# Performance work log

Hardware: AMD Instinct MI355X
Metric: run time of the kernel (lower is better)

## Reference

```python
import jax, jax.numpy as jnp
import numpy as np

V, N, D, HEADS = 4, 1536, 256, 4


def setup_inputs() -> dict:
    key = jax.random.key(0)
    ks = jax.random.split(key, 8)
    s = 0.05  # weight init scale
    return {
        "H": jax.random.normal(ks[0], (V, N, D), jnp.float32),
        "C": jax.random.normal(ks[1], (V, V, N, N), jnp.float32),
        "WQ": jax.random.normal(ks[2], (V, D, D), jnp.float32) * s,
        "WK": jax.random.normal(ks[3], (V, D, D), jnp.float32) * s,
        "WV": jax.random.normal(ks[4], (V, D, D), jnp.float32) * s,
        "in_proj_w": jax.random.normal(ks[5], (3 * D, D), jnp.float32) * s,
        "in_proj_b": jnp.zeros((3 * D,), jnp.float32),
        "out_proj_w": jax.random.normal(ks[6], (D, D), jnp.float32) * s,
        "out_proj_b": jnp.zeros((D,), jnp.float32),
        "alphas": jnp.full((V,), 0.95, jnp.float32),
        "alpha_align": jnp.asarray(0.5, jnp.float32),
        "beta": jnp.asarray(0.5, jnp.float32),
        "topk": 32,
    }


def _ircva(H, in_proj_w, in_proj_b, out_proj_w, out_proj_b, alphas):
    # torch MultiheadAttention, seq=V, batch=N, embed=D, heads=HEADS
    dh = D // HEADS
    qkv = jnp.einsum('snd,ed->sne', H, in_proj_w) + in_proj_b  # (V,N,3D)
    q, k, v = jnp.split(qkv, 3, axis=-1)
    q = q.reshape(V, N, HEADS, dh)
    k = k.reshape(V, N, HEADS, dh)
    v = v.reshape(V, N, HEADS, dh)
    att = jnp.einsum('snhd,tnhd->nhst', q, k) / jnp.sqrt(jnp.float32(dh))
    w = jax.nn.softmax(att, axis=-1)
    o = jnp.einsum('nhst,tnhd->snhd', w, v).reshape(V, N, D)
    fusion = jnp.einsum('snd,ed->sne', o, out_proj_w) + out_proj_b
    a = alphas[:, None, None]
    return fusion * a + (1.0 - a) * H  # (V,N,D)


def _crcva(aligned, C, WQ, WK, WV, K):
    # per-view projections: Linear y = x @ W.T
    Qn = jnp.einsum('vnd,ved->vne', aligned, WQ)
    Kn = jnp.einsum('vnd,ved->vne', aligned, WK)
    Vn = jnp.einsum('vnd,ved->vne', aligned, WV)
    # per-row top-k sparsification of C[p,q]
    vals, idx = jax.lax.top_k(C, K)  # (V,V,N,K)
    Cf = C.reshape(-1, N)
    rows = jnp.arange(Cf.shape[0])[:, None]
    sparse = jnp.zeros_like(Cf).at[rows, idx.reshape(-1, K)].set(vals.reshape(-1, K))
    sparse = sparse.reshape(V, V, N, N)
    row_sum = sparse.sum(axis=-1, keepdims=True) + 1e-12
    C_hat = sparse / row_sum
    # diagonal (p==q) pairs are left as zeros in the torch code
    offdiag = (1.0 - jnp.eye(V, dtype=C.dtype))[:, :, None, None]
    C_hat = C_hat * offdiag
    mask = (C_hat > 0).astype(C.dtype)
    scores = jnp.einsum('pnd,qmd->pqnm', Qn, Kn) / jnp.sqrt(jnp.float32(D))
    scores = scores * mask + (1.0 - mask) * (-1e9)
    alpha_nbr = jax.nn.softmax(scores, axis=-1)
    return jnp.einsum('pqnm,qmd->pnd', alpha_nbr, Vn)  # (V,N,D)


def reference(H, C, WQ, WK, WV, in_proj_w, in_proj_b, out_proj_w, out_proj_b,
              alphas, alpha_align, beta, topk):
    aligned = _ircva(H, in_proj_w, in_proj_b, out_proj_w, out_proj_b, alphas)
    nbr = _crcva(aligned, C, WQ, WK, WV, int(topk))
    a = jax.nn.sigmoid(alpha_align)
    f_fuse = jax.nn.relu(a * aligned + (1.0 - a) * nbr)
    return beta * H + (1.0 - beta) * f_fuse  # (V,N,D)
```

## Files before the change

kernel.cpp:

```cpp
#include <hip/hip_runtime.h>
#include <hip/hip_bf16.h>
#include <math.h>

typedef __bf16 bf16x8 __attribute__((ext_vector_type(8)));
typedef __bf16 bf16x4 __attribute__((ext_vector_type(4)));
typedef float  f32x4  __attribute__((ext_vector_type(4)));

static constexpr int kV = 4;
static constexpr int kN = 1536;
static constexpr int kD = 256;
static constexpr int kTopK = 32;

__global__ __launch_bounds__(256) void convert_kernel(
    const float* __restrict__ H, const float* __restrict__ inW,
    const float* __restrict__ outW, const float* __restrict__ WQ,
    const float* __restrict__ WK, const float* __restrict__ WV,
    __bf16* __restrict__ Hb, __bf16* __restrict__ inWb,
    __bf16* __restrict__ outWb, __bf16* __restrict__ Wqkvb,
    float* __restrict__ Vmean)
{
    if (blockIdx.x == 0) {
        f32x4 z = {0.f, 0.f, 0.f, 0.f};
        *(f32x4*)(Vmean + threadIdx.x * 4) = z;
    }
    int idx = (blockIdx.x * 256 + threadIdx.x) * 4;
    const float* src; __bf16* dst; int off;
    if      (idx < 1572864) { src = H;    dst = Hb;             off = idx; }
    else if (idx < 1769472) { src = inW;  dst = inWb;           off = idx - 1572864; }
    else if (idx < 1835008) { src = outW; dst = outWb;          off = idx - 1769472; }
    else if (idx < 2097152) { src = WQ;   dst = Wqkvb;          off = idx - 1835008; }
    else if (idx < 2359296) { src = WK;   dst = Wqkvb + 262144; off = idx - 2097152; }
    else                    { src = WV;   dst = Wqkvb + 524288; off = idx - 2359296; }
    f32x4 v = *(const f32x4*)(src + off);
    bf16x4 b;
#pragma unroll
    for (int j = 0; j < 4; ++j) b[j] = (__bf16)v[j];
    *(bf16x4*)(dst + off) = b;
}

__global__ __launch_bounds__(256) void gemm_qkv_kernel(
    const __bf16* __restrict__ A, const __bf16* __restrict__ Bm,
    const float* __restrict__ bias, __bf16* __restrict__ outB)
{
    const int Nc = 768, K = 256;
    int wave = blockIdx.x * 4 + (threadIdx.x >> 6);
    int tm  = wave / 12;
    int tn4 = wave - tm * 12;
    int lane = threadIdx.x & 63;
    int r    = lane & 15;
    int quad = lane >> 4;
    const __bf16* Ap = A + (size_t)(tm * 32 + r) * K + quad * 8;
    const __bf16* Bp = Bm + (size_t)(tn4 * 64 + r) * K + quad * 8;
    f32x4 acc[2][4] = {};
    for (int k0 = 0; k0 < K; k0 += 32) {
        bf16x8 a0 = *(const bf16x8*)(Ap + k0);
        bf16x8 a1 = *(const bf16x8*)(Ap + (size_t)16 * K + k0);
#pragma unroll
        for (int t = 0; t < 4; ++t) {
            bf16x8 b = *(const bf16x8*)(Bp + (size_t)t * 16 * K + k0);
            acc[0][t] = __builtin_amdgcn_mfma_f32_16x16x32_bf16(a0, b, acc[0][t], 0, 0, 0);
            acc[1][t] = __builtin_amdgcn_mfma_f32_16x16x32_bf16(a1, b, acc[1][t], 0, 0, 0);
        }
    }
#pragma unroll
    for (int t = 0; t < 4; ++t) {
        int gn = tn4 * 64 + t * 16 + r;
        float bv = bias[gn];
#pragma unroll
        for (int mt = 0; mt < 2; ++mt)
#pragma unroll
            for (int i = 0; i < 4; ++i) {
                int gm = tm * 32 + mt * 16 + quad * 4 + i;
                outB[(size_t)gm * Nc + gn] = (__bf16)(acc[mt][t][i] + bv);
            }
    }
}

__global__ __launch_bounds__(256) void attg3_kernel(
    const __bf16* __restrict__ qkv, const __bf16* __restrict__ outWb,
    const float* __restrict__ outBias, const float* __restrict__ H,
    const float* __restrict__ alphas,
    float* __restrict__ alignedF, __bf16* __restrict__ alignedB)
{
    __shared__ __bf16 obuf[16][280];
    int n0 = blockIdx.x * 4;
    int tid = threadIdx.x;
    int h = tid >> 6, d = tid & 63;
#pragma unroll
    for (int ni = 0; ni < 4; ++ni) {
        int n = n0 + ni;
        float q[4], k[4], vv[4];
#pragma unroll
        for (int s = 0; s < 4; ++s) {
            size_t base = (size_t)(s * kN + n) * 768 + h * 64 + d;
            q[s]  = (float)qkv[base];
            k[s]  = (float)qkv[base + 256];
            vv[s] = (float)qkv[base + 512];
        }
        float att[4][4];
#pragma unroll
        for (int s = 0; s < 4; ++s)
#pragma unroll
            for (int t = 0; t < 4; ++t) {
                float p = q[s] * k[t];
#pragma unroll
                for (int off = 32; off > 0; off >>= 1) p += __shfl_xor(p, off);
                att[s][t] = p * 0.125f;
            }
#pragma unroll
        for (int s = 0; s < 4; ++s) {
            float mx = fmaxf(fmaxf(att[s][0], att[s][1]), fmaxf(att[s][2], att[s][3]));
            float e0 = __expf(att[s][0] - mx), e1 = __expf(att[s][1] - mx);
            float e2 = __expf(att[s][2] - mx), e3 = __expf(att[s][3] - mx);
            float inv = 1.f / (e0 + e1 + e2 + e3);
            float ov = (e0 * vv[0] + e1 * vv[1] + e2 * vv[2] + e3 * vv[3]) * inv;
            obuf[s * 4 + ni][h * 64 + d] = (__bf16)ov;
        }
    }
    __syncthreads();
    int w = tid >> 6, lane = tid & 63;
    int r = lane & 15, quad = lane >> 4;
    f32x4 acc[4] = {};
    for (int k0 = 0; k0 < 256; k0 += 32) {
        bf16x8 a = *(const bf16x8*)&obuf[r][quad * 8 + k0];
#pragma unroll
        for (int t = 0; t < 4; ++t) {
            bf16x8 b = *(const bf16x8*)(outWb + (size_t)(w * 64 + t * 16 + r) * 256 + quad * 8 + k0);
            acc[t] = __builtin_amdgcn_mfma_f32_16x16x32_bf16(a, b, acc[t], 0, 0, 0);
        }
    }
#pragma unroll
    for (int t = 0; t < 4; ++t) {
        int gn = w * 64 + t * 16 + r;
        float bv = outBias[gn];
#pragma unroll
        for (int i = 0; i < 4; ++i) {
            int rl = quad * 4 + i;
            int s = rl >> 2, ni = rl & 3;
            size_t gr = (size_t)(s * kN + n0 + ni);
            float a_ = alphas[s];
            size_t off = gr * kD + gn;
            float res = a_ * (acc[t][i] + bv) + (1.f - a_) * H[off];
            alignedF[off] = res;
            alignedB[off] = (__bf16)res;
        }
    }
}

__global__ __launch_bounds__(256) void gemm_qkv3_kernel(
    const __bf16* __restrict__ A, const __bf16* __restrict__ W,
    __bf16* __restrict__ O0, __bf16* __restrict__ O1, __bf16* __restrict__ O2,
    float* __restrict__ Vmean)
{
    int proj = blockIdx.y;
    __bf16* Ob = (proj == 0) ? O0 : (proj == 1) ? O1 : O2;
    const __bf16* Wb = W + (size_t)proj * 4 * 65536;
    int b = blockIdx.x;
    int view = b / 48;
    int tn4 = threadIdx.x >> 6;
    int lane = threadIdx.x & 63;
    int r = lane & 15, quad = lane >> 4;
    const __bf16* Ap = A + (size_t)(b * 32 + r) * kD + quad * 8;
    const __bf16* Bp = Wb + (size_t)view * 65536 + (size_t)(tn4 * 64 + r) * kD + quad * 8;
    f32x4 acc[2][4] = {};
    for (int k0 = 0; k0 < kD; k0 += 32) {
        bf16x8 a0 = *(const bf16x8*)(Ap + k0);
        bf16x8 a1 = *(const bf16x8*)(Ap + (size_t)16 * kD + k0);
#pragma unroll
        for (int t = 0; t < 4; ++t) {
            bf16x8 bb = *(const bf16x8*)(Bp + (size_t)t * 16 * kD + k0);
            acc[0][t] = __builtin_amdgcn_mfma_f32_16x16x32_bf16(a0, bb, acc[0][t], 0, 0, 0);
            acc[1][t] = __builtin_amdgcn_mfma_f32_16x16x32_bf16(a1, bb, acc[1][t], 0, 0, 0);
        }
    }
#pragma unroll
    for (int t = 0; t < 4; ++t) {
        int gn = tn4 * 64 + t * 16 + r;
#pragma unroll
        for (int mt = 0; mt < 2; ++mt)
#pragma unroll
            for (int i = 0; i < 4; ++i) {
                int gm = b * 32 + mt * 16 + quad * 4 + i;
                Ob[(size_t)gm * kD + gn] = (__bf16)acc[mt][t][i];
            }
    }
    if (proj == 2) {
#pragma unroll
        for (int t = 0; t < 4; ++t) {
            float cs = 0.f;
#pragma unroll
            for (int mt = 0; mt < 2; ++mt)
#pragma unroll
                for (int i = 0; i < 4; ++i) cs += acc[mt][t][i];
            cs += __shfl_xor(cs, 16);
            cs += __shfl_xor(cs, 32);
            if (quad == 0)
                atomicAdd(&Vmean[view * kD + tn4 * 64 + t * 16 + r], cs * (1.f / 1536.f));
        }
    }
}

__global__ __launch_bounds__(256) void crcva_kernel(
    const float* __restrict__ C,
    const __bf16* __restrict__ Qn, const __bf16* __restrict__ Kn,
    const __bf16* __restrict__ Vn, const float* __restrict__ Vmean,
    const float* __restrict__ alignedF, const float* __restrict__ H,
    const float* __restrict__ alpha_align, const float* __restrict__ beta,
    float* __restrict__ out)
{
    int gid = blockIdx.x;
    int j8  = gid & 7;
    int p   = j8 & 3;
    int n   = ((gid >> 3) << 1) | (j8 >> 2);
    int tid = threadIdx.x;
    int w = tid >> 6, lane = tid & 63;
    __shared__ unsigned int hist[3][257];
    __shared__ unsigned int sbin[3];
    __shared__ unsigned int idxl[3][kTopK];
    __shared__ unsigned int scnt[3];
    __shared__ float qsh[kD];
    __shared__ float wsh[96];
    __shared__ int   osh[96];
    __shared__ float part[4][kD];

    size_t eoff = ((size_t)p * kN + n) * kD + tid;
    float pre_al = alignedF[eoff];
    float pre_h  = H[eoff];
    float pre_vm = Vmean[p * kD + tid];
    float pre_aa = alpha_align[0];
    float pre_bt = beta[0];

    if (w < 3) {
        int q = w + (w >= p ? 1 : 0);
        const float* row = C + ((size_t)((p * kV + q) * kN + n)) * kN;
        unsigned int key[24];
#pragma unroll
        for (int j = 0; j < 6; ++j) {
            f32x4 v4 = __builtin_nontemporal_load((const f32x4*)(row + j * 256 + lane * 4));
#pragma unroll
            for (int e = 0; e < 4; ++e) {
                unsigned int u = __float_as_uint(v4[e]);
                key[j * 4 + e] = (u & 0x80000000u) ? ~u : (u | 0x80000000u);
            }
        }
        if (lane == 0) scnt[w] = 0;
        const unsigned int T0 = 0xBFCCCCCDu;
        unsigned int cand = 0;
#pragma unroll
        for (int j = 0; j < 24; ++j) cand |= (key[j] > T0) ? (1u << j) : 0u;
        unsigned int myc = (unsigned int)__popc(cand);
#pragma unroll
        for (int off = 1; off < 64; off <<= 1) myc += __shfl_xor(myc, off);
        if (myc < kTopK) {
            cand = 0;
#pragma unroll
            for (int j = 0; j < 24; ++j) cand |= (key[j] > 0x80000000u) ? (1u << j) : 0u;
        }
        unsigned int pref = 0, need = kTopK;
#pragma unroll
        for (int pass = 0; pass < 4; ++pass) {
            const int shift = 24 - 8 * pass;
#pragma unroll
            for (int k2 = 0; k2 < 4; ++k2) hist[w][lane * 4 + k2] = 0;
            if (lane == 0) sbin[w] = 0;
            __builtin_amdgcn_wave_barrier();
#pragma unroll
            for (int j = 0; j < 24; ++j) {
                unsigned int k = key[j];
                bool match = ((cand >> j) & 1u) &&
                             ((pass == 0) || (((k ^ pref) >> (shift + 8)) == 0));
                if (match) atomicAdd(&hist[w][(k >> shift) & 255u], 1u);
            }
            __builtin_amdgcn_wave_barrier();
            unsigned int h0 = hist[w][lane*4+0], h1 = hist[w][lane*4+1];
            unsigned int h2 = hist[w][lane*4+2], h3 = hist[w][lane*4+3];
            unsigned int s3 = h3, s2 = h2 + s3, s1 = h1 + s2, s0 = h0 + s1;
            unsigned int run = s0;
#pragma unroll
            for (int off = 1; off < 64; off <<= 1) {
                unsigned int v = __shfl_down(run, off);
                if (lane + off < 64) run += v;
            }
            if (pass == 0) {
                unsigned int tot = __shfl(run, 0);
                need = need < tot ? need : tot;
            }
            unsigned int above = run - s0;
            unsigned int suf[4]  = {above+s0, above+s1, above+s2, above+s3};
            unsigned int sufN[4] = {above+s1, above+s2, above+s3, above};
#pragma unroll
            for (int k2 = 0; k2 < 4; ++k2)
                if (suf[k2] >= need && sufN[k2] < need)
                    sbin[w] = ((unsigned int)(lane*4 + k2) << 16) | sufN[k2];
            __builtin_amdgcn_wave_barrier();
            unsigned int pk = sbin[w];
            pref |= (pk >> 16) << shift;
            need -= (pk & 0xffffu);
            __builtin_amdgcn_wave_barrier();
        }
        unsigned int T = pref;
        unsigned int eq = 0;
#pragma unroll
        for (int j = 0; j < 24; ++j)
            eq += (((cand >> j) & 1u) && key[j] == T) ? 1u : 0u;
#pragma unroll
        for (int off = 1; off < 64; off <<= 1) eq += __shfl_xor(eq, off);
        if (eq == need) {
#pragma unroll
            for (int j = 0; j < 24; ++j) {
                if (((cand >> j) & 1u) && key[j] >= T) {
                    unsigned int pos = atomicAdd(&scnt[w], 1u);
                    idxl[w][pos] = (unsigned int)((j >> 2) * 256 + lane * 4 + (j & 3));
                }
            }
        } else {
            unsigned int eqBefore = 0;
            unsigned long long below = (1ull << lane) - 1ull;
            for (int j4 = 0; j4 < 6; ++j4) {
                unsigned long long m[4];
#pragma unroll
                for (int e = 0; e < 4; ++e)
                    m[e] = __ballot(((cand >> (j4*4+e)) & 1u) && key[j4 * 4 + e] == T);
#pragma unroll
                for (int e = 0; e < 4; ++e) {
                    unsigned int k = key[j4 * 4 + e];
                    bool inc = (cand >> (j4*4+e)) & 1u;
                    unsigned int rank = eqBefore;
#pragma unroll
                    for (int e2 = 0; e2 < 4; ++e2) rank += (unsigned int)__popcll(m[e2] & below);
                    for (int e2 = 0; e2 < e; ++e2) rank += (unsigned int)((m[e2] >> lane) & 1ull);
                    bool iseq = inc && (k == T);
                    bool take = (inc && k > T) || (iseq && rank < need);
                    if (take) {
                        unsigned int pos = atomicAdd(&scnt[w], 1u);
                        idxl[w][pos] = (unsigned int)(j4 * 256 + lane * 4 + e);
                    }
                }
                eqBefore += (unsigned int)(__popcll(m[0]) + __popcll(m[1])
                                         + __popcll(m[2]) + __popcll(m[3]));
            }
        }
    } else {
        bf16x4 qv = *(const bf16x4*)(Qn + ((size_t)p * kN + n) * kD + lane * 4);
#pragma unroll
        for (int e = 0; e < 4; ++e) qsh[lane * 4 + e] = (float)qv[e];
    }
    __syncthreads();

    if (tid < 192) {
        int j = tid >> 1, half = tid & 1;
        int g = j >> 5, r = j & 31;
        int q = g + (g >= p ? 1 : 0);
        int cnt = (int)scnt[g];
        bool valid = (r < cnt);
        int m = valid ? (int)idxl[g][r] : 0;
        int off = valid ? (q * kN + m) * kD : 0;
        float s = 0.f;
        if (valid) {
            const __bf16* kr = Kn + off + half * 128;
            const float*  qh = qsh + half * 128;
            float a0 = 0.f, a1 = 0.f, a2 = 0.f, a3 = 0.f;
#pragma unroll
            for (int dd = 0; dd < 128; dd += 32) {
                bf16x8 k0 = *(const bf16x8*)(kr + dd);
                bf16x8 k1 = *(const bf16x8*)(kr + dd + 8);
                bf16x8 k2 = *(const bf16x8*)(kr + dd + 16);
                bf16x8 k3 = *(const bf16x8*)(kr + dd + 24);
                const float* q0 = qh + dd;
#pragma unroll
                for (int e = 0; e < 8; ++e) {
                    a0 += q0[e]      * (float)k0[e];
                    a1 += q0[e + 8]  * (float)k1[e];
                    a2 += q0[e + 16] * (float)k2[e];
                    a3 += q0[e + 24] * (float)k3[e];
                }
            }
            s = (a0 + a1) + (a2 + a3);
        }
        s += __shfl_xor(s, 1);
        float sc = valid ? s * 0.0625f : -1e30f;
        float mx = sc;
#pragma unroll
        for (int o2 = 2; o2 <= 32; o2 <<= 1) mx = fmaxf(mx, __shfl_xor(mx, o2));
        float e = valid ? __expf(sc - mx) : 0.f;
        float ss = e;
#pragma unroll
        for (int o2 = 2; o2 <= 32; o2 <<= 1) ss += __shfl_xor(ss, o2);
        if (half == 0) {
            wsh[j] = (ss > 0.f) ? e / ss : 0.f;
            osh[j] = off;
        }
    }
    __syncthreads();

    {
        int half32 = lane >> 5, l32 = lane & 31;
        float a[8] = {};
#pragma unroll
        for (int it = 0; it < 12; ++it) {
            int j = w * 24 + it * 2 + half32;
            float wt = wsh[j];
            bf16x8 v = *(const bf16x8*)(Vn + osh[j] + l32 * 8);
#pragma unroll
            for (int e = 0; e < 8; ++e) a[e] += wt * (float)v[e];
        }
#pragma unroll
        for (int e = 0; e < 8; ++e) a[e] += __shfl_xor(a[e], 32);
        if (half32 == 0) {
#pragma unroll
            for (int e = 0; e < 8; ++e) part[w][l32 * 8 + e] = a[e];
        }
    }
    __syncthreads();

    float acc = pre_vm + part[0][tid] + part[1][tid] + part[2][tid] + part[3][tid];
    float aa = 1.f / (1.f + __expf(-pre_aa));
    float f  = fmaxf(aa * pre_al + (1.f - aa) * acc, 0.f);
    out[eoff] = pre_h * pre_bt + (1.f - pre_bt) * f;
}

extern "C" void kernel_launch(void* const* d_in, const int* in_sizes, int n_in,
                              void* d_out, int out_size, void* d_ws, size_t ws_size,
                              hipStream_t stream)
{
    const float* H        = (const float*)d_in[0];
    const float* C        = (const float*)d_in[1];
    const float* WQ       = (const float*)d_in[2];
    const float* WK       = (const float*)d_in[3];
    const float* WV       = (const float*)d_in[4];
    const float* inW      = (const float*)d_in[5];
    const float* inB      = (const float*)d_in[6];
    const float* outW     = (const float*)d_in[7];
    const float* outBias  = (const float*)d_in[8];
    const float* alphas   = (const float*)d_in[9];
    const float* alpha_al = (const float*)d_in[10];
    const float* beta     = (const float*)d_in[11];
    float* out = (float*)d_out;

    char* w = (char*)d_ws;
    __bf16* Hb       = (__bf16*)w;  w += (size_t)6144 * 256 * 2;
    __bf16* inWb     = (__bf16*)w;  w += (size_t)768 * 256 * 2;
    __bf16* outWb    = (__bf16*)w;  w += (size_t)256 * 256 * 2;
    __bf16* Wqkvb    = (__bf16*)w;  w += (size_t)3 * 4 * 256 * 256 * 2;
    __bf16* qkv      = (__bf16*)w;  w += (size_t)6144 * 768 * 2;
    __bf16* alignedB = (__bf16*)w;  w += (size_t)6144 * 256 * 2;
    float*  alignedF = (float*)w;   w += (size_t)6144 * 256 * 4;
    __bf16* Qn       = (__bf16*)w;  w += (size_t)6144 * 256 * 2;
    __bf16* Kn       = (__bf16*)w;  w += (size_t)6144 * 256 * 2;
    __bf16* Vn       = (__bf16*)w;  w += (size_t)6144 * 256 * 2;
    float*  Vmean    = (float*)w;   w += (size_t)4 * 256 * 4;

    convert_kernel<<<2560, 256, 0, stream>>>(H, inW, outW, WQ, WK, WV,
                                             Hb, inWb, outWb, Wqkvb, Vmean);
    gemm_qkv_kernel<<<576, 256, 0, stream>>>(Hb, inWb, inB, qkv);
    attg3_kernel<<<384, 256, 0, stream>>>(qkv, outWb, outBias, H, alphas,
                                          alignedF, alignedB);
    gemm_qkv3_kernel<<<dim3(192, 3), 256, 0, stream>>>(alignedB, Wqkvb,
                                                       Qn, Kn, Vn, Vmean);
    crcva_kernel<<<6144, 256, 0, stream>>>(C, Qn, Kn, Vn, Vmean,
        alignedF, H, alpha_al, beta, out);
}
```

Measured before the change: 363.0 us.

## Compact top-k candidates into LDS and store K/V projections as fp32

The radix-select top-k now has a fast path. When the threshold-filtered candidate count falls between 32 and 150, candidates are compacted into shared memory with a ballot prefix scan, so each histogram pass touches about three entries per lane instead of scanning all 24 keys. The pass also records the winning bin count, which replaces a separate equality-count reduction. K and V projections are stored as fp32 instead of bf16, which drops the conversions in the gather dot products and the V accumulation. The cost is double the gather traffic for K/V, plus extra shared memory that may lower occupancy.

```diff
diff --git a/kernel.cpp b/kernel.cpp
--- a/kernel.cpp
+++ b/kernel.cpp
@@ -149,11 +149,10 @@
 
 __global__ __launch_bounds__(256) void gemm_qkv3_kernel(
     const __bf16* __restrict__ A, const __bf16* __restrict__ W,
-    __bf16* __restrict__ O0, __bf16* __restrict__ O1, __bf16* __restrict__ O2,
+    __bf16* __restrict__ Qn, float* __restrict__ KnF, float* __restrict__ VnF,
     float* __restrict__ Vmean)
 {
     int proj = blockIdx.y;
-    __bf16* Ob = (proj == 0) ? O0 : (proj == 1) ? O1 : O2;
     const __bf16* Wb = W + (size_t)proj * 4 * 65536;
     int b = blockIdx.x;
     int view = b / 48;
@@ -173,6 +172,7 @@
             acc[1][t] = __builtin_amdgcn_mfma_f32_16x16x32_bf16(a1, bb, acc[1][t], 0, 0, 0);
         }
     }
+    float* OF = (proj == 1) ? KnF : VnF;
 #pragma unroll
     for (int t = 0; t < 4; ++t) {
         int gn = tn4 * 64 + t * 16 + r;
@@ -181,7 +181,8 @@
 #pragma unroll
             for (int i = 0; i < 4; ++i) {
                 int gm = b * 32 + mt * 16 + quad * 4 + i;
-                Ob[(size_t)gm * kD + gn] = (__bf16)acc[mt][t][i];
+                if (proj == 0) Qn[(size_t)gm * kD + gn] = (__bf16)acc[mt][t][i];
+                else           OF[(size_t)gm * kD + gn] = acc[mt][t][i];
             }
     }
     if (proj == 2) {
@@ -202,8 +203,8 @@
 
 __global__ __launch_bounds__(256) void crcva_kernel(
     const float* __restrict__ C,
-    const __bf16* __restrict__ Qn, const __bf16* __restrict__ Kn,
-    const __bf16* __restrict__ Vn, const float* __restrict__ Vmean,
+    const __bf16* __restrict__ Qn, const float* __restrict__ KnF,
+    const float* __restrict__ VnF, const float* __restrict__ Vmean,
     const float* __restrict__ alignedF, const float* __restrict__ H,
     const float* __restrict__ alpha_align, const float* __restrict__ beta,
     float* __restrict__ out)
@@ -218,6 +219,8 @@
     __shared__ unsigned int sbin[3];
     __shared__ unsigned int idxl[3][kTopK];
     __shared__ unsigned int scnt[3];
+    __shared__ unsigned int ckey[3][152];
+    __shared__ unsigned int cidx[3][152];
     __shared__ float qsh[kD];
     __shared__ float wsh[96];
     __shared__ int   osh[96];
@@ -240,7 +243,7 @@
 #pragma unroll
             for (int e = 0; e < 4; ++e) {
                 unsigned int u = __float_as_uint(v4[e]);
-                key[j * 4 + e] = (u & 0x80000000u) ? ~u : (u | 0x80000000u);
+                key[j * 4 + e] = u ^ ((unsigned int)((int)u >> 31) | 0x80000000u);
             }
         }
         if (lane == 0) scnt[w] = 0;
@@ -251,93 +254,180 @@
         unsigned int myc = (unsigned int)__popc(cand);
 #pragma unroll
         for (int off = 1; off < 64; off <<= 1) myc += __shfl_xor(myc, off);
-        if (myc < kTopK) {
-            cand = 0;
-#pragma unroll
-            for (int j = 0; j < 24; ++j) cand |= (key[j] > 0x80000000u) ? (1u << j) : 0u;
-        }
-        unsigned int pref = 0, need = kTopK;
-#pragma unroll
-        for (int pass = 0; pass < 4; ++pass) {
-            const int shift = 24 - 8 * pass;
-#pragma unroll
-            for (int k2 = 0; k2 < 4; ++k2) hist[w][lane * 4 + k2] = 0;
-            if (lane == 0) sbin[w] = 0;
+        bool fastsel = (myc >= kTopK && myc <= 150);
+        unsigned int pref = 0, need = kTopK, h3win = 0;
+        unsigned long long below = (1ull << lane) - 1ull;
+        if (fastsel) {
+            unsigned int ccnt = 0;
+#pragma unroll
+            for (int j = 0; j < 24; ++j) {
+                bool b = (cand >> j) & 1u;
+                unsigned long long m = __ballot(b);
+                if (b) {
+                    unsigned int pos = ccnt + (unsigned int)__popcll(m & below);
+                    ckey[w][pos] = key[j];
+                    cidx[w][pos] = (unsigned int)((j >> 2) * 256 + lane * 4 + (j & 3));
+                }
+                ccnt += (unsigned int)__popcll(m);
+            }
             __builtin_amdgcn_wave_barrier();
 #pragma unroll
-            for (int j = 0; j < 24; ++j) {
-                unsigned int k = key[j];
-                bool match = ((cand >> j) & 1u) &&
-                             ((pass == 0) || (((k ^ pref) >> (shift + 8)) == 0));
-                if (match) atomicAdd(&hist[w][(k >> shift) & 255u], 1u);
-            }
-            __builtin_amdgcn_wave_barrier();
-            unsigned int h0 = hist[w][lane*4+0], h1 = hist[w][lane*4+1];
-            unsigned int h2 = hist[w][lane*4+2], h3 = hist[w][lane*4+3];
-            unsigned int s3 = h3, s2 = h2 + s3, s1 = h1 + s2, s0 = h0 + s1;
-            unsigned int run = s0;
-#pragma unroll
-            for (int off = 1; off < 64; off <<= 1) {
-                unsigned int v = __shfl_down(run, off);
-                if (lane + off < 64) run += v;
-            }
-            if (pass == 0) {
-                unsigned int tot = __shfl(run, 0);
-                need = need < tot ? need : tot;
-            }
-            unsigned int above = run - s0;
-            unsigned int suf[4]  = {above+s0, above+s1, above+s2, above+s3};
-            unsigned int sufN[4] = {above+s1, above+s2, above+s3, above};
-#pragma unroll
-            for (int k2 = 0; k2 < 4; ++k2)
-                if (suf[k2] >= need && sufN[k2] < need)
-                    sbin[w] = ((unsigned int)(lane*4 + k2) << 16) | sufN[k2];
-            __builtin_amdgcn_wave_barrier();
-            unsigned int pk = sbin[w];
-            pref |= (pk >> 16) << shift;
-            need -= (pk & 0xffffu);
-            __builtin_amdgcn_wave_barrier();
-        }
-        unsigned int T = pref;
-        unsigned int eq = 0;
-#pragma unroll
-        for (int j = 0; j < 24; ++j)
-            eq += (((cand >> j) & 1u) && key[j] == T) ? 1u : 0u;
-#pragma unroll
-        for (int off = 1; off < 64; off <<= 1) eq += __shfl_xor(eq, off);
-        if (eq == need) {
-#pragma unroll
-            for (int j = 0; j < 24; ++j) {
-                if (((cand >> j) & 1u) && key[j] >= T) {
-                    unsigned int pos = atomicAdd(&scnt[w], 1u);
-                    idxl[w][pos] = (unsigned int)((j >> 2) * 256 + lane * 4 + (j & 3));
+            for (int pass = 0; pass < 4; ++pass) {
+                const int shift = 24 - 8 * pass;
+#pragma unroll
+                for (int k2 = 0; k2 < 4; ++k2) hist[w][lane * 4 + k2] = 0;
+                __builtin_amdgcn_wave_barrier();
+#pragma unroll
+                for (int s = 0; s < 3; ++s) {
+                    int i = lane + s * 64;
+                    if (i < (int)ccnt) {
+                        unsigned int k = ckey[w][i];
+                        if (pass == 0 || ((k ^ pref) >> (shift + 8)) == 0)
+                            atomicAdd(&hist[w][(k >> shift) & 255u], 1u);
+                    }
+                }
+                __builtin_amdgcn_wave_barrier();
+                unsigned int h0 = hist[w][lane*4+0], h1 = hist[w][lane*4+1];
+                unsigned int h2 = hist[w][lane*4+2], h3 = hist[w][lane*4+3];
+                unsigned int s3 = h3, s2 = h2 + s3, s1 = h1 + s2, s0 = h0 + s1;
+                unsigned int run = s0;
+#pragma unroll
+                for (int off = 1; off < 64; off <<= 1) {
+                    unsigned int v = __shfl_down(run, off);
+                    if (lane + off < 64) run += v;
+                }
+                unsigned int above = run - s0;
+                unsigned int suf[4]  = {above+s0, above+s1, above+s2, above+s3};
+                unsigned int sufN[4] = {above+s1, above+s2, above+s3, above};
+#pragma unroll
+                for (int k2 = 0; k2 < 4; ++k2)
+                    if (suf[k2] >= need && sufN[k2] < need)
+                        sbin[w] = ((unsigned int)(lane*4 + k2) << 22)
+                                | ((suf[k2] - sufN[k2]) << 11) | sufN[k2];
+                __builtin_amdgcn_wave_barrier();
+                unsigned int pk = sbin[w];
+                pref |= (pk >> 22) << shift;
+                need -= (pk & 0x7FFu);
+                if (pass == 3) h3win = (pk >> 11) & 0x7FFu;
+                __builtin_amdgcn_wave_barrier();
+            }
+            unsigned int T = pref;
+            if (h3win == need) {
+#pragma unroll
+                for (int s = 0; s < 3; ++s) {
+                    int i = lane + s * 64;
+                    if (i < (int)ccnt && ckey[w][i] >= T) {
+                        unsigned int pos = atomicAdd(&scnt[w], 1u);
+                        idxl[w][pos] = cidx[w][i];
+                    }
+                }
+            } else {
+                unsigned int eqBefore = 0;
+                for (int j4 = 0; j4 < 6; ++j4) {
+                    unsigned long long m[4];
+#pragma unroll
+                    for (int e = 0; e < 4; ++e)
+                        m[e] = __ballot(((cand >> (j4*4+e)) & 1u) && key[j4*4+e] == T);
+#pragma unroll
+                    for (int e = 0; e < 4; ++e) {
+                        unsigned int k = key[j4 * 4 + e];
+                        bool inc = (cand >> (j4*4+e)) & 1u;
+                        unsigned int rank = eqBefore;
+#pragma unroll
+                        for (int e2 = 0; e2 < 4; ++e2) rank += (unsigned int)__popcll(m[e2] & below);
+                        for (int e2 = 0; e2 < e; ++e2) rank += (unsigned int)((m[e2] >> lane) & 1ull);
+                        bool take = (inc && k > T) || (inc && k == T && rank < need);
+                        if (take) {
+                            unsigned int pos = atomicAdd(&scnt[w], 1u);
+                            idxl[w][pos] = (unsigned int)(j4 * 256 + lane * 4 + e);
+                        }
+                    }
+                    eqBefore += (unsigned int)(__popcll(m[0]) + __popcll(m[1])
+                                             + __popcll(m[2]) + __popcll(m[3]));
                 }
             }
         } else {
-            unsigned int eqBefore = 0;
-            unsigned long long below = (1ull << lane) - 1ull;
-            for (int j4 = 0; j4 < 6; ++j4) {
-                unsigned long long m[4];
-#pragma unroll
-                for (int e = 0; e < 4; ++e)
-                    m[e] = __ballot(((cand >> (j4*4+e)) & 1u) && key[j4 * 4 + e] == T);
-#pragma unroll
-                for (int e = 0; e < 4; ++e) {
-                    unsigned int k = key[j4 * 4 + e];
-                    bool inc = (cand >> (j4*4+e)) & 1u;
-                    unsigned int rank = eqBefore;
-#pragma unroll
-                    for (int e2 = 0; e2 < 4; ++e2) rank += (unsigned int)__popcll(m[e2] & below);
-                    for (int e2 = 0; e2 < e; ++e2) rank += (unsigned int)((m[e2] >> lane) & 1ull);
-                    bool iseq = inc && (k == T);
-                    bool take = (inc && k > T) || (iseq && rank < need);
-                    if (take) {
+            if (myc < kTopK) {
+                cand = 0;
+#pragma unroll
+                for (int j = 0; j < 24; ++j) cand |= (key[j] > 0x80000000u) ? (1u << j) : 0u;
+            }
+            need = kTopK;
+#pragma unroll
+            for (int pass = 0; pass < 4; ++pass) {
+                const int shift = 24 - 8 * pass;
+#pragma unroll
+                for (int k2 = 0; k2 < 4; ++k2) hist[w][lane * 4 + k2] = 0;
+                __builtin_amdgcn_wave_barrier();
+#pragma unroll
+                for (int j = 0; j < 24; ++j) {
+                    unsigned int k = key[j];
+                    bool match = ((cand >> j) & 1u) &&
+                                 ((pass == 0) || (((k ^ pref) >> (shift + 8)) == 0));
+                    if (match) atomicAdd(&hist[w][(k >> shift) & 255u], 1u);
+                }
+                __builtin_amdgcn_wave_barrier();
+                unsigned int h0 = hist[w][lane*4+0], h1 = hist[w][lane*4+1];
+                unsigned int h2 = hist[w][lane*4+2], h3 = hist[w][lane*4+3];
+                unsigned int s3 = h3, s2 = h2 + s3, s1 = h1 + s2, s0 = h0 + s1;
+                unsigned int run = s0;
+#pragma unroll
+                for (int off = 1; off < 64; off <<= 1) {
+                    unsigned int v = __shfl_down(run, off);
+                    if (lane + off < 64) run += v;
+                }
+                if (pass == 0) {
+                    unsigned int tot = __shfl(run, 0);
+                    need = need < tot ? need : tot;
+                }
+                unsigned int above = run - s0;
+                unsigned int suf[4]  = {above+s0, above+s1, above+s2, above+s3};
+                unsigned int sufN[4] = {above+s1, above+s2, above+s3, above};
+#pragma unroll
+                for (int k2 = 0; k2 < 4; ++k2)
+                    if (suf[k2] >= need && sufN[k2] < need)
+                        sbin[w] = ((unsigned int)(lane*4 + k2) << 22)
+                                | ((suf[k2] - sufN[k2]) << 11) | sufN[k2];
+                __builtin_amdgcn_wave_barrier();
+                unsigned int pk = sbin[w];
+                pref |= (pk >> 22) << shift;
+                need -= (pk & 0x7FFu);
+                if (pass == 3) h3win = (pk >> 11) & 0x7FFu;
+                __builtin_amdgcn_wave_barrier();
+            }
+            unsigned int T = pref;
+            if (h3win == need) {
+#pragma unroll
+                for (int j = 0; j < 24; ++j) {
+                    if (((cand >> j) & 1u) && key[j] >= T) {
                         unsigned int pos = atomicAdd(&scnt[w], 1u);
-                        idxl[w][pos] = (unsigned int)(j4 * 256 + lane * 4 + e);
+                        idxl[w][pos] = (unsigned int)((j >> 2) * 256 + lane * 4 + (j & 3));
                     }
                 }
-                eqBefore += (unsigned int)(__popcll(m[0]) + __popcll(m[1])
-                                         + __popcll(m[2]) + __popcll(m[3]));
+            } else {
+                unsigned int eqBefore = 0;
+                for (int j4 = 0; j4 < 6; ++j4) {
+                    unsigned long long m[4];
+#pragma unroll
+                    for (int e = 0; e < 4; ++e)
+                        m[e] = __ballot(((cand >> (j4*4+e)) & 1u) && key[j4*4+e] == T);
+#pragma unroll
+                    for (int e = 0; e < 4; ++e) {
+                        unsigned int k = key[j4 * 4 + e];
+                        bool inc = (cand >> (j4*4+e)) & 1u;
+                        unsigned int rank = eqBefore;
+#pragma unroll
+                        for (int e2 = 0; e2 < 4; ++e2) rank += (unsigned int)__popcll(m[e2] & below);
+                        for (int e2 = 0; e2 < e; ++e2) rank += (unsigned int)((m[e2] >> lane) & 1ull);
+                        bool take = (inc && k > T) || (inc && k == T && rank < need);
+                        if (take) {
+                            unsigned int pos = atomicAdd(&scnt[w], 1u);
+                            idxl[w][pos] = (unsigned int)(j4 * 256 + lane * 4 + e);
+                        }
+                    }
+                    eqBefore += (unsigned int)(__popcll(m[0]) + __popcll(m[1])
+                                             + __popcll(m[2]) + __popcll(m[3]));
+                }
             }
         }
     } else {
@@ -357,23 +447,20 @@
         int off = valid ? (q * kN + m) * kD : 0;
         float s = 0.f;
         if (valid) {
-            const __bf16* kr = Kn + off + half * 128;
-            const float*  qh = qsh + half * 128;
+            const float* kr = KnF + off + half * 128;
+            const float* qh = qsh + half * 128;
             float a0 = 0.f, a1 = 0.f, a2 = 0.f, a3 = 0.f;
 #pragma unroll
-            for (int dd = 0; dd < 128; dd += 32) {
-                bf16x8 k0 = *(const bf16x8*)(kr + dd);
-                bf16x8 k1 = *(const bf16x8*)(kr + dd + 8);
-                bf16x8 k2 = *(const bf16x8*)(kr + dd + 16);
-                bf16x8 k3 = *(const bf16x8*)(kr + dd + 24);
+            for (int dd = 0; dd < 128; dd += 16) {
+                f32x4 k0 = *(const f32x4*)(kr + dd);
+                f32x4 k1 = *(const f32x4*)(kr + dd + 4);
+                f32x4 k2 = *(const f32x4*)(kr + dd + 8);
+                f32x4 k3 = *(const f32x4*)(kr + dd + 12);
                 const float* q0 = qh + dd;
-#pragma unroll
-                for (int e = 0; e < 8; ++e) {
-                    a0 += q0[e]      * (float)k0[e];
-                    a1 += q0[e + 8]  * (float)k1[e];
-                    a2 += q0[e + 16] * (float)k2[e];
-                    a3 += q0[e + 24] * (float)k3[e];
-                }
+                a0 += q0[0]*k0[0] + q0[1]*k0[1] + q0[2]*k0[2] + q0[3]*k0[3];
+                a1 += q0[4]*k1[0] + q0[5]*k1[1] + q0[6]*k1[2] + q0[7]*k1[3];
+                a2 += q0[8]*k2[0] + q0[9]*k2[1] + q0[10]*k2[2] + q0[11]*k2[3];
+                a3 += q0[12]*k3[0] + q0[13]*k3[1] + q0[14]*k3[2] + q0[15]*k3[3];
             }
             s = (a0 + a1) + (a2 + a3);
         }
@@ -394,22 +481,16 @@
     __syncthreads();
 
     {
-        int half32 = lane >> 5, l32 = lane & 31;
-        float a[8] = {};
-#pragma unroll
-        for (int it = 0; it < 12; ++it) {
-            int j = w * 24 + it * 2 + half32;
+        float a0 = 0.f, a1 = 0.f, a2 = 0.f, a3 = 0.f;
+#pragma unroll
+        for (int jj = 0; jj < 24; ++jj) {
+            int j = w * 24 + jj;
             float wt = wsh[j];
-            bf16x8 v = *(const bf16x8*)(Vn + osh[j] + l32 * 8);
-#pragma unroll
-            for (int e = 0; e < 8; ++e) a[e] += wt * (float)v[e];
-        }
-#pragma unroll
-        for (int e = 0; e < 8; ++e) a[e] += __shfl_xor(a[e], 32);
-        if (half32 == 0) {
-#pragma unroll
-            for (int e = 0; e < 8; ++e) part[w][l32 * 8 + e] = a[e];
-        }
+            f32x4 v = *(const f32x4*)(VnF + osh[j] + lane * 4);
+            a0 += wt * v[0]; a1 += wt * v[1]; a2 += wt * v[2]; a3 += wt * v[3];
+        }
+        f32x4 av = {a0, a1, a2, a3};
+        *(f32x4*)&part[w][lane * 4] = av;
     }
     __syncthreads();
 
@@ -446,8 +527,8 @@
     __bf16* alignedB = (__bf16*)w;  w += (size_t)6144 * 256 * 2;
     float*  alignedF = (float*)w;   w += (size_t)6144 * 256 * 4;
     __bf16* Qn       = (__bf16*)w;  w += (size_t)6144 * 256 * 2;
-    __bf16* Kn       = (__bf16*)w;  w += (size_t)6144 * 256 * 2;
-    __bf16* Vn       = (__bf16*)w;  w += (size_t)6144 * 256 * 2;
+    float*  KnF      = (float*)w;   w += (size_t)6144 * 256 * 4;
+    float*  VnF      = (float*)w;   w += (size_t)6144 * 256 * 4;
     float*  Vmean    = (float*)w;   w += (size_t)4 * 256 * 4;
 
     convert_kernel<<<2560, 256, 0, stream>>>(H, inW, outW, WQ, WK, WV,
@@ -456,7 +537,7 @@
     attg3_kernel<<<384, 256, 0, stream>>>(qkv, outWb, outBias, H, alphas,
                                           alignedF, alignedB);
     gemm_qkv3_kernel<<<dim3(192, 3), 256, 0, stream>>>(alignedB, Wqkvb,
-                                                       Qn, Kn, Vn, Vmean);
-    crcva_kernel<<<6144, 256, 0, stream>>>(C, Qn, Kn, Vn, Vmean,
+                                                       Qn, KnF, VnF, Vmean);
+    crcva_kernel<<<6144, 256, 0, stream>>>(C, Qn, KnF, VnF, Vmean,
         alignedF, H, alpha_al, beta, out);
 }
```

New measurement: 431.3 us. 18.8% more time.
